# Kernel tuning notes

Hardware: AMD Instinct MI355X
Metric: run time of the kernel (lower is better)

Reference implementation:

```python
import jax, jax.numpy as jnp
import numpy as np


def setup_inputs() -> dict:
    key = jax.random.key(0)
    ks = jax.random.split(key, 5)
    B, S, D, U = 4, 2048, 1024, 1024
    scale = 1.0 / np.sqrt(D)
    return {
        "query": jax.random.normal(ks[0], (B, S, D), dtype=jnp.float32),
        "value": jax.random.normal(ks[1], (B, S, D), dtype=jnp.float32),
        "Wq": jax.random.normal(ks[2], (D, U), dtype=jnp.float32) * scale,
        "bq": jnp.zeros((U,), dtype=jnp.float32),
        "Wk": jax.random.normal(ks[3], (D, U), dtype=jnp.float32) * scale,
        "bk": jnp.zeros((U,), dtype=jnp.float32),
        "Wv": jax.random.normal(ks[4], (D, U), dtype=jnp.float32) * scale,
        "bv": jnp.zeros((U,), dtype=jnp.float32),
    }


def reference(query, value, Wq, bq, Wk, bk, Wv, bv):
    # Dense projections (last-dim matmul + bias)
    Q = jnp.einsum("bsd,du->bsu", query, Wq) + bq   # [B,Sq,U]
    K = jnp.einsum("btd,du->btu", value, Wk) + bk   # [B,Sk,U]
    V = jnp.einsum("btd,du->btu", value, Wv) + bv   # [B,Sk,U]
    d_k = jnp.asarray(K.shape[-1], dtype=jnp.float32)
    scores = jnp.einsum("bsu,btu->bst", Q, K) / jnp.sqrt(d_k)  # [B,Sq,Sk]
    weights = jax.nn.softmax(scores, axis=-1)
    return jnp.einsum("bst,btu->bsu", weights, V)   # [B,Sq,U]
```

## Files before the change

kernel.cpp:

```cpp
#include <hip/hip_runtime.h>
#include <hip/hip_bf16.h>
#include <stdint.h>

#define DEVINL __device__ __forceinline__

typedef __attribute__((ext_vector_type(4))) float f32x4;
typedef __attribute__((ext_vector_type(8))) __bf16 bfv8;
typedef __attribute__((ext_vector_type(8))) short s16x8;
typedef __attribute__((ext_vector_type(4))) short s16x4;

DEVINL short f2bf(float f) {
  union { float f; unsigned u; } v; v.f = f;
  unsigned r = v.u + 0x7FFFu + ((v.u >> 16) & 1u);
  return (short)(r >> 16);
}
DEVINL float bf2f(short h) {
  union { unsigned u; float f; } v; v.u = ((unsigned)(unsigned short)h) << 16;
  return v.f;
}
DEVINL void gload_lds16(const void* g, void* l) {
  __builtin_amdgcn_global_load_lds((__attribute__((address_space(1))) unsigned*)(g),
                                   (__attribute__((address_space(3))) unsigned*)(l),
                                   16, 0, 0);
}
template <int N> DEVINL void vmwaitc() {
  asm volatile("s_waitcnt vmcnt(%0)" :: "i"(N) : "memory");
}
DEVINL int xswz(int p, int n) { return (p & 7) * (n >> 3) + (p >> 3); }

DEVINL void gemm97_core(const short* __restrict__ Ag, const short* __restrict__ Bg,
                        int lda, int ldb, int m0, int n0, int nkt,
                        short* lds, f32x4 (&acc)[4][4]) {
  const int tid = threadIdx.x;
  const int w = tid >> 6, l = tid & 63;
  const int wm = w >> 1, wn = w & 1;
  const int lr = l & 15, lg = l >> 4;
  const int ck = ((lg ^ ((lr >> 1) & 3)) << 3);
  const int aro = (wm * 64 + lr) * 32 + ck;
  const int bro = 4096 + (wn * 64 + lr) * 32 + ck;
  const int srow = l >> 2;
  const int scol = (((l & 3) ^ ((l >> 3) & 3)) << 3);

#pragma unroll 1
  for (int kt = 0; kt < nkt; ++kt) {
#pragma unroll
    for (int i = 0; i < 2; ++i) {
      gload_lds16(Ag + (size_t)(m0 + w * 32 + i * 16 + srow) * lda + kt * 32 + scol,
                  lds + w * 1024 + i * 512);
      gload_lds16(Bg + (size_t)(n0 + w * 32 + i * 16 + srow) * ldb + kt * 32 + scol,
                  lds + 4096 + w * 1024 + i * 512);
    }
    vmwaitc<0>();
    __syncthreads();
    bfv8 af[4], bfr[4];
#pragma unroll
    for (int mf = 0; mf < 4; ++mf) af[mf] = *(const bfv8*)(lds + aro + mf * 512);
#pragma unroll
    for (int nf = 0; nf < 4; ++nf) bfr[nf] = *(const bfv8*)(lds + bro + nf * 512);
#pragma unroll
    for (int mf = 0; mf < 4; ++mf)
#pragma unroll
      for (int nf = 0; nf < 4; ++nf)
        acc[mf][nf] = __builtin_amdgcn_mfma_f32_16x16x32_bf16(af[mf], bfr[nf], acc[mf][nf], 0, 0, 0);
    __syncthreads();
  }
}

__global__ __launch_bounds__(256) void prep_kernel(
    const float* __restrict__ q, const float* __restrict__ v,
    const float* __restrict__ Wq, const float* __restrict__ Wk, const float* __restrict__ Wv,
    short* __restrict__ Qc, short* __restrict__ Vc,
    short* __restrict__ WTq, short* __restrict__ WTk, short* __restrict__ WTv) {
  __shared__ float tile[64][65];
  const int bx = blockIdx.x;
  if (bx < 8192) {
    const float* src = (bx < 4096) ? q : v;
    short* dst = (bx < 4096) ? Qc : Vc;
    const size_t i = ((size_t)(bx & 4095) * 256 + threadIdx.x) * 8;
    f32x4 x0 = *(const f32x4*)(src + i);
    f32x4 x1 = *(const f32x4*)(src + i + 4);
    s16x8 o;
#pragma unroll
    for (int j = 0; j < 4; ++j) { o[j] = f2bf(x0[j]); o[4 + j] = f2bf(x1[j]); }
    *(s16x8*)(dst + i) = o;
  } else {
    const int z = (bx - 8192) >> 8, xx = (bx - 8192) & 255;
    const float* W = (z == 0) ? Wq : (z == 1) ? Wk : Wv;
    short* WT = (z == 0) ? WTq : (z == 1) ? WTk : WTv;
    const int k0 = (xx & 15) << 6, n0 = (xx >> 4) << 6;
    const int c = threadIdx.x & 63, r0 = threadIdx.x >> 6;
#pragma unroll
    for (int i = 0; i < 16; ++i) {
      int r = (i << 2) + r0;
      tile[r][c] = W[(size_t)(k0 + r) * 1024 + n0 + c];
    }
    __syncthreads();
#pragma unroll
    for (int i = 0; i < 16; ++i) {
      int a = (i << 2) + r0;
      WT[(size_t)(n0 + a) * 1024 + k0 + c] = f2bf(tile[c][a]);
    }
  }
}

__global__ __launch_bounds__(256, 3) void qkproj_kernel(
    const short* __restrict__ Qc, const short* __restrict__ Vc,
    const short* __restrict__ WTq, const short* __restrict__ WTk,
    const float* __restrict__ bq, const float* __restrict__ bk,
    short* __restrict__ Qb, short* __restrict__ Kb) {
  __shared__ short lds[8192];
  const int o = xswz(blockIdx.x, 1024);
  const int sel = o >> 9, r = o & 511;
  const int bm = r >> 3, bn = r & 7;
  const short* A = sel ? Vc : Qc;
  const short* BT = sel ? WTk : WTq;
  const float* bias = sel ? bk : bq;
  short* O = sel ? Kb : Qb;
  const int m0 = bm * 128, n0 = bn * 128;
  f32x4 acc[4][4];
#pragma unroll
  for (int i = 0; i < 4; ++i)
#pragma unroll
    for (int j = 0; j < 4; ++j) acc[i][j] = (f32x4){0.f, 0.f, 0.f, 0.f};
  gemm97_core(A, BT, 1024, 1024, m0, n0, 32, lds, acc);
  const int l = threadIdx.x & 63, w = threadIdx.x >> 6;
  const int wm = w >> 1, wn = w & 1, lr = l & 15, lg = l >> 4;
#pragma unroll
  for (int mf = 0; mf < 4; ++mf) {
    const int row0 = m0 + wm * 64 + mf * 16 + lg * 4;
#pragma unroll
    for (int nf = 0; nf < 4; ++nf) {
      const int col = n0 + wn * 64 + nf * 16 + lr;
      const float bb = bias[col];
#pragma unroll
      for (int j = 0; j < 4; ++j)
        O[(size_t)(row0 + j) * 1024 + col] = f2bf(acc[mf][nf][j] + bb);
    }
  }
}

__global__ __launch_bounds__(256, 3) void vproj_kernel(
    const short* __restrict__ Vc, const short* __restrict__ WTv,
    const float* __restrict__ bv, short* __restrict__ VT) {
  __shared__ short lds[8704];
  const int o = xswz(blockIdx.x, 512);
  const int bm = o >> 3, bn = o & 7;
  const int m0 = bm * 128, n0 = bn * 128;
  f32x4 acc[4][4];
#pragma unroll
  for (int i = 0; i < 4; ++i)
#pragma unroll
    for (int j = 0; j < 4; ++j) acc[i][j] = (f32x4){0.f, 0.f, 0.f, 0.f};
  gemm97_core(Vc, WTv, 1024, 1024, m0, n0, 32, lds, acc);
  const int tid = threadIdx.x;
  const int l = tid & 63, w = tid >> 6;
  const int wm = w >> 1, wn = w & 1, lr = l & 15, lg = l >> 4;
  const int b = m0 >> 11, t0 = m0 & 2047;
#pragma unroll 1
  for (int h = 0; h < 2; ++h) {
    if (wn == h) {
#pragma unroll
      for (int mf = 0; mf < 4; ++mf) {
        const int tl = wm * 64 + mf * 16 + lg * 4;
#pragma unroll
        for (int nf = 0; nf < 4; ++nf) {
          const int ul = nf * 16 + lr;
          const float bb = bv[n0 + h * 64 + ul];
          s16x4 pk;
#pragma unroll
          for (int j = 0; j < 4; ++j) pk[j] = f2bf(acc[mf][nf][j] + bb);
          *(s16x4*)&lds[ul * 136 + tl] = pk;
        }
      }
    }
    __syncthreads();
#pragma unroll
    for (int it = 0; it < 4; ++it) {
      const int cid = it * 256 + tid;
      const int u = cid >> 4, tc = cid & 15;
      s16x8 v8 = *(const s16x8*)&lds[u * 136 + tc * 8];
      *(s16x8*)(VT + ((size_t)b * 1024 + n0 + h * 64 + u) * 2048 + t0 + tc * 8) = v8;
    }
    __syncthreads();
  }
}

__global__ __launch_bounds__(256, 3) void qkt_kernel(const short* __restrict__ Qb,
                                                     const short* __restrict__ Kb,
                                                     short* __restrict__ Sb) {
  __shared__ short lds[8192];
  const int o = xswz(blockIdx.x, 1024);
  const int bt = o >> 8, r = o & 255;
  const int bm = r >> 4, bn = r & 15;
  const short* A = Qb + (size_t)bt * 2097152;
  const short* B = Kb + (size_t)bt * 2097152;
  short* O = Sb + (size_t)bt * 4194304;
  const int m0 = bm * 128, n0 = bn * 128;
  f32x4 acc[4][4];
#pragma unroll
  for (int i = 0; i < 4; ++i)
#pragma unroll
    for (int j = 0; j < 4; ++j) acc[i][j] = (f32x4){0.f, 0.f, 0.f, 0.f};
  gemm97_core(A, B, 1024, 1024, m0, n0, 32, lds, acc);
  const int l = threadIdx.x & 63, w = threadIdx.x >> 6;
  const int wm = w >> 1, wn = w & 1, lr = l & 15, lg = l >> 4;
#pragma unroll
  for (int mf = 0; mf < 4; ++mf) {
    const int row0 = m0 + wm * 64 + mf * 16 + lg * 4;
#pragma unroll
    for (int nf = 0; nf < 4; ++nf) {
      const int col = n0 + wn * 64 + nf * 16 + lr;
#pragma unroll
      for (int j = 0; j < 4; ++j)
        O[(size_t)(row0 + j) * 2048 + col] = f2bf(acc[mf][nf][j] * 0.03125f);
    }
  }
}

__global__ __launch_bounds__(256, 3) void pv_kernel(const short* __restrict__ Sb,
                                                    const short* __restrict__ VT,
                                                    float* __restrict__ Out) {
  __shared__ short lds[8192];
  const int o = xswz(blockIdx.x, 512);
  const int bt = o >> 7, r = o & 127;
  const int bm = r >> 3, bn = r & 7;
  const short* A = Sb + (size_t)bt * 4194304;
  const short* B = VT + (size_t)bt * 2097152;
  float* O = Out + (size_t)bt * 2097152;
  const int m0 = bm * 128, n0 = bn * 128;
  f32x4 acc[4][4];
#pragma unroll
  for (int i = 0; i < 4; ++i)
#pragma unroll
    for (int j = 0; j < 4; ++j) acc[i][j] = (f32x4){0.f, 0.f, 0.f, 0.f};
  gemm97_core(A, B, 2048, 2048, m0, n0, 64, lds, acc);
  const int l = threadIdx.x & 63, w = threadIdx.x >> 6;
  const int wm = w >> 1, wn = w & 1, lr = l & 15, lg = l >> 4;
#pragma unroll
  for (int mf = 0; mf < 4; ++mf) {
    const int row0 = m0 + wm * 64 + mf * 16 + lg * 4;
#pragma unroll
    for (int nf = 0; nf < 4; ++nf) {
      const int col = n0 + wn * 64 + nf * 16 + lr;
#pragma unroll
      for (int j = 0; j < 4; ++j)
        O[(size_t)(row0 + j) * 1024 + col] = acc[mf][nf][j];
    }
  }
}

__global__ __launch_bounds__(256) void softmax_kernel(short* __restrict__ Sb) {
  const size_t row = blockIdx.x;
  short* p = Sb + row * 2048;
  const int tid = threadIdx.x;
  const int w = tid >> 6, l = tid & 63;
  s16x8 v = *(const s16x8*)(p + tid * 8);
  float f[8];
#pragma unroll
  for (int j = 0; j < 8; ++j) f[j] = bf2f(v[j]);
  float m = f[0];
#pragma unroll
  for (int j = 1; j < 8; ++j) m = fmaxf(m, f[j]);
#pragma unroll
  for (int o = 32; o > 0; o >>= 1) m = fmaxf(m, __shfl_xor(m, o, 64));
  __shared__ float redm[4], reds[4];
  if (l == 0) redm[w] = m;
  __syncthreads();
  m = fmaxf(fmaxf(redm[0], redm[1]), fmaxf(redm[2], redm[3]));
  float s = 0.f;
#pragma unroll
  for (int j = 0; j < 8; ++j) { f[j] = __expf(f[j] - m); s += f[j]; }
#pragma unroll
  for (int o = 32; o > 0; o >>= 1) s += __shfl_xor(s, o, 64);
  if (l == 0) reds[w] = s;
  __syncthreads();
  s = reds[0] + reds[1] + reds[2] + reds[3];
  const float inv = 1.f / s;
  s16x8 o8;
#pragma unroll
  for (int j = 0; j < 8; ++j) o8[j] = f2bf(f[j] * inv);
  *(s16x8*)(p + tid * 8) = o8;
}

extern "C" void kernel_launch(void* const* d_in, const int* in_sizes, int n_in,
                              void* d_out, int out_size, void* d_ws, size_t ws_size,
                              hipStream_t stream) {
  const float* query = (const float*)d_in[0];
  const float* value = (const float*)d_in[1];
  const float* Wq = (const float*)d_in[2];
  const float* bq = (const float*)d_in[3];
  const float* Wk = (const float*)d_in[4];
  const float* bk = (const float*)d_in[5];
  const float* Wv = (const float*)d_in[6];
  const float* bv = (const float*)d_in[7];

  char* ws = (char*)d_ws;
  short* WTq = (short*)(ws);
  short* WTk = (short*)(ws + ((size_t)2 << 20));
  short* WTv = (short*)(ws + ((size_t)4 << 20));
  short* Qc  = (short*)(ws + ((size_t)6 << 20));
  short* Vc  = (short*)(ws + ((size_t)22 << 20));
  short* Sb  = (short*)(ws + ((size_t)6 << 20));
  short* Qb  = (short*)(ws + ((size_t)38 << 20));
  short* Kb  = (short*)(ws + ((size_t)54 << 20));
  short* VT  = (short*)(ws + ((size_t)70 << 20));

  prep_kernel<<<dim3(8960), 256, 0, stream>>>(query, value, Wq, Wk, Wv, Qc, Vc, WTq, WTk, WTv);

  qkproj_kernel<<<dim3(1024), 256, 0, stream>>>(Qc, Vc, WTq, WTk, bq, bk, Qb, Kb);
  vproj_kernel<<<dim3(512), 256, 0, stream>>>(Vc, WTv, bv, VT);

  qkt_kernel<<<dim3(1024), 256, 0, stream>>>(Qb, Kb, Sb);

  softmax_kernel<<<dim3(8192), 256, 0, stream>>>(Sb);

  pv_kernel<<<dim3(512), 256, 0, stream>>>(Sb, VT, (float*)d_out);
}
```

Measured before the change: 198.6 us.

## Fold Wq·Wkᵀ into one matrix to drop the K projection GEMM

Rewrites the score computation as X·(Wq·Wkᵀ)·Yᵀ, precomputing the 1024x1024 product once and removing the separate K projection. The bq term becomes a per-key vector, computed only when bq is nonzero, and bk is dropped since softmax is invariant to per-row constants. This removes one large projection GEMM at the cost of a small extra GEMM, an extra rounding of the fused matrix to bf16, and a reshuffled workspace layout.

```diff
diff --git a/kernel.cpp b/kernel.cpp
--- a/kernel.cpp
+++ b/kernel.cpp
@@ -70,13 +70,16 @@
     const float* __restrict__ q, const float* __restrict__ v,
     const float* __restrict__ Wq, const float* __restrict__ Wk, const float* __restrict__ Wv,
     short* __restrict__ Qc, short* __restrict__ Vc,
-    short* __restrict__ WTq, short* __restrict__ WTk, short* __restrict__ WTv) {
+    short* __restrict__ Wqc, short* __restrict__ Wkc, short* __restrict__ WTv) {
   __shared__ float tile[64][65];
   const int bx = blockIdx.x;
-  if (bx < 8192) {
-    const float* src = (bx < 4096) ? q : v;
-    short* dst = (bx < 4096) ? Qc : Vc;
-    const size_t i = ((size_t)(bx & 4095) * 256 + threadIdx.x) * 8;
+  if (bx < 9216) {
+    const float* src; short* dst; int off;
+    if (bx < 4096)      { src = q;  dst = Qc;  off = bx; }
+    else if (bx < 8192) { src = v;  dst = Vc;  off = bx - 4096; }
+    else if (bx < 8704) { src = Wq; dst = Wqc; off = bx - 8192; }
+    else                { src = Wk; dst = Wkc; off = bx - 8704; }
+    const size_t i = ((size_t)off * 256 + threadIdx.x) * 8;
     f32x4 x0 = *(const f32x4*)(src + i);
     f32x4 x1 = *(const f32x4*)(src + i + 4);
     s16x8 o;
@@ -84,45 +87,68 @@
     for (int j = 0; j < 4; ++j) { o[j] = f2bf(x0[j]); o[4 + j] = f2bf(x1[j]); }
     *(s16x8*)(dst + i) = o;
   } else {
-    const int z = (bx - 8192) >> 8, xx = (bx - 8192) & 255;
-    const float* W = (z == 0) ? Wq : (z == 1) ? Wk : Wv;
-    short* WT = (z == 0) ? WTq : (z == 1) ? WTk : WTv;
+    const int xx = bx - 9216;
     const int k0 = (xx & 15) << 6, n0 = (xx >> 4) << 6;
     const int c = threadIdx.x & 63, r0 = threadIdx.x >> 6;
 #pragma unroll
     for (int i = 0; i < 16; ++i) {
       int r = (i << 2) + r0;
-      tile[r][c] = W[(size_t)(k0 + r) * 1024 + n0 + c];
+      tile[r][c] = Wv[(size_t)(k0 + r) * 1024 + n0 + c];
     }
     __syncthreads();
 #pragma unroll
     for (int i = 0; i < 16; ++i) {
       int a = (i << 2) + r0;
-      WT[(size_t)(n0 + a) * 1024 + k0 + c] = f2bf(tile[c][a]);
-    }
-  }
-}
-
-__global__ __launch_bounds__(256, 3) void qkproj_kernel(
-    const short* __restrict__ Qc, const short* __restrict__ Vc,
-    const short* __restrict__ WTq, const short* __restrict__ WTk,
-    const float* __restrict__ bq, const float* __restrict__ bk,
-    short* __restrict__ Qb, short* __restrict__ Kb) {
+      WTv[(size_t)(n0 + a) * 1024 + k0 + c] = f2bf(tile[c][a]);
+    }
+  }
+}
+
+__global__ __launch_bounds__(256) void bias0_kernel(const float* __restrict__ Wk,
+                                                    const float* __restrict__ bq,
+                                                    float* __restrict__ v1,
+                                                    float* __restrict__ flagp) {
+  __shared__ float red[256];
+  const int t = threadIdx.x;
+  float any = 0.f;
+  for (int i = t; i < 1024; i += 256) any += fabsf(bq[i]);
+  red[t] = any; __syncthreads();
+  for (int s = 128; s > 0; s >>= 1) { if (t < s) red[t] += red[t + s]; __syncthreads(); }
+  const float fl = red[0];
+  if (t == 0) *flagp = fl;
+  if (fl != 0.f) {
+    for (int r = t; r < 1024; r += 256) {
+      float acc = 0.f;
+      for (int u = 0; u < 1024; ++u) acc += Wk[(size_t)r * 1024 + u] * bq[u];
+      v1[r] = acc;
+    }
+  }
+}
+
+__global__ __launch_bounds__(256) void tvec_kernel(const float* __restrict__ Y,
+                                                   const float* __restrict__ v1,
+                                                   const float* __restrict__ flagp,
+                                                   float* __restrict__ tvec) {
+  const int t = blockIdx.x * 256 + threadIdx.x;
+  if (*flagp == 0.f) { tvec[t] = 0.f; return; }
+  float acc = 0.f;
+  for (int d = 0; d < 1024; ++d) acc += Y[(size_t)t * 1024 + d] * v1[d];
+  tvec[t] = acc;
+}
+
+__global__ __launch_bounds__(256, 3) void mker_kernel(const short* __restrict__ Wkc,
+                                                      const short* __restrict__ Wqc,
+                                                      short* __restrict__ MT) {
   __shared__ short lds[8192];
-  const int o = xswz(blockIdx.x, 1024);
-  const int sel = o >> 9, r = o & 511;
-  const int bm = r >> 3, bn = r & 7;
-  const short* A = sel ? Vc : Qc;
-  const short* BT = sel ? WTk : WTq;
-  const float* bias = sel ? bk : bq;
-  short* O = sel ? Kb : Qb;
-  const int m0 = bm * 128, n0 = bn * 128;
-  f32x4 acc[4][4];
-#pragma unroll
-  for (int i = 0; i < 4; ++i)
-#pragma unroll
-    for (int j = 0; j < 4; ++j) acc[i][j] = (f32x4){0.f, 0.f, 0.f, 0.f};
-  gemm97_core(A, BT, 1024, 1024, m0, n0, 32, lds, acc);
+  const int o = xswz(blockIdx.x, 64);
+  const int bm = o >> 3, bn = o & 7;
+  const int m0 = bm * 128, n0 = bn * 128;
+  f32x4 acc[4][4];
+#pragma unroll
+  for (int i = 0; i < 4; ++i)
+#pragma unroll
+    for (int j = 0; j < 4; ++j) acc[i][j] = (f32x4){0.f, 0.f, 0.f, 0.f};
+  gemm97_core(Wkc, Wqc, 1024, 1024, m0, n0, 32, lds, acc);
   const int l = threadIdx.x & 63, w = threadIdx.x >> 6;
   const int wm = w >> 1, wn = w & 1, lr = l & 15, lg = l >> 4;
 #pragma unroll
@@ -131,10 +157,37 @@
 #pragma unroll
     for (int nf = 0; nf < 4; ++nf) {
       const int col = n0 + wn * 64 + nf * 16 + lr;
-      const float bb = bias[col];
 #pragma unroll
       for (int j = 0; j < 4; ++j)
-        O[(size_t)(row0 + j) * 1024 + col] = f2bf(acc[mf][nf][j] + bb);
+        MT[(size_t)(row0 + j) * 1024 + col] = f2bf(acc[mf][nf][j]);
+    }
+  }
+}
+
+__global__ __launch_bounds__(256, 3) void qproj_kernel(const short* __restrict__ Qc,
+                                                       const short* __restrict__ MT,
+                                                       short* __restrict__ Ap) {
+  __shared__ short lds[8192];
+  const int o = xswz(blockIdx.x, 512);
+  const int bm = o >> 3, bn = o & 7;
+  const int m0 = bm * 128, n0 = bn * 128;
+  f32x4 acc[4][4];
+#pragma unroll
+  for (int i = 0; i < 4; ++i)
+#pragma unroll
+    for (int j = 0; j < 4; ++j) acc[i][j] = (f32x4){0.f, 0.f, 0.f, 0.f};
+  gemm97_core(Qc, MT, 1024, 1024, m0, n0, 32, lds, acc);
+  const int l = threadIdx.x & 63, w = threadIdx.x >> 6;
+  const int wm = w >> 1, wn = w & 1, lr = l & 15, lg = l >> 4;
+#pragma unroll
+  for (int mf = 0; mf < 4; ++mf) {
+    const int row0 = m0 + wm * 64 + mf * 16 + lg * 4;
+#pragma unroll
+    for (int nf = 0; nf < 4; ++nf) {
+      const int col = n0 + wn * 64 + nf * 16 + lr;
+#pragma unroll
+      for (int j = 0; j < 4; ++j)
+        Ap[(size_t)(row0 + j) * 1024 + col] = f2bf(acc[mf][nf][j]);
     }
   }
 }
@@ -185,16 +238,18 @@
   }
 }
 
-__global__ __launch_bounds__(256, 3) void qkt_kernel(const short* __restrict__ Qb,
-                                                     const short* __restrict__ Kb,
-                                                     short* __restrict__ Sb) {
+__global__ __launch_bounds__(256, 3) void qkt_kernel(const short* __restrict__ Ap,
+                                                     const short* __restrict__ Vc,
+                                                     const float* __restrict__ tvec,
+                                                     short* __restrict__ sb0,
+                                                     short* __restrict__ sb3) {
   __shared__ short lds[8192];
   const int o = xswz(blockIdx.x, 1024);
   const int bt = o >> 8, r = o & 255;
   const int bm = r >> 4, bn = r & 15;
-  const short* A = Qb + (size_t)bt * 2097152;
-  const short* B = Kb + (size_t)bt * 2097152;
-  short* O = Sb + (size_t)bt * 4194304;
+  const short* A = Ap + (size_t)bt * 2097152;
+  const short* B = Vc + (size_t)bt * 2097152;
+  short* O = (bt < 3) ? (sb0 + (size_t)bt * 4194304) : sb3;
   const int m0 = bm * 128, n0 = bn * 128;
   f32x4 acc[4][4];
 #pragma unroll
@@ -205,26 +260,28 @@
   const int l = threadIdx.x & 63, w = threadIdx.x >> 6;
   const int wm = w >> 1, wn = w & 1, lr = l & 15, lg = l >> 4;
 #pragma unroll
-  for (int mf = 0; mf < 4; ++mf) {
-    const int row0 = m0 + wm * 64 + mf * 16 + lg * 4;
-#pragma unroll
-    for (int nf = 0; nf < 4; ++nf) {
-      const int col = n0 + wn * 64 + nf * 16 + lr;
+  for (int nf = 0; nf < 4; ++nf) {
+    const int col = n0 + wn * 64 + nf * 16 + lr;
+    const float tv = tvec[bt * 2048 + col];
+#pragma unroll
+    for (int mf = 0; mf < 4; ++mf) {
+      const int row0 = m0 + wm * 64 + mf * 16 + lg * 4;
 #pragma unroll
       for (int j = 0; j < 4; ++j)
-        O[(size_t)(row0 + j) * 2048 + col] = f2bf(acc[mf][nf][j] * 0.03125f);
-    }
-  }
-}
-
-__global__ __launch_bounds__(256, 3) void pv_kernel(const short* __restrict__ Sb,
+        O[(size_t)(row0 + j) * 2048 + col] = f2bf((acc[mf][nf][j] + tv) * 0.03125f);
+    }
+  }
+}
+
+__global__ __launch_bounds__(256, 3) void pv_kernel(const short* __restrict__ sb0,
+                                                    const short* __restrict__ sb3,
                                                     const short* __restrict__ VT,
                                                     float* __restrict__ Out) {
   __shared__ short lds[8192];
   const int o = xswz(blockIdx.x, 512);
   const int bt = o >> 7, r = o & 127;
   const int bm = r >> 3, bn = r & 7;
-  const short* A = Sb + (size_t)bt * 4194304;
+  const short* A = (bt < 3) ? (sb0 + (size_t)bt * 4194304) : sb3;
   const short* B = VT + (size_t)bt * 2097152;
   float* O = Out + (size_t)bt * 2097152;
   const int m0 = bm * 128, n0 = bn * 128;
@@ -249,9 +306,11 @@
   }
 }
 
-__global__ __launch_bounds__(256) void softmax_kernel(short* __restrict__ Sb) {
-  const size_t row = blockIdx.x;
-  short* p = Sb + row * 2048;
+__global__ __launch_bounds__(256) void softmax_kernel(short* __restrict__ sb0,
+                                                      short* __restrict__ sb3) {
+  const int row = blockIdx.x;
+  const int bt = row >> 11;
+  short* p = ((bt < 3) ? (sb0 + (size_t)bt * 4194304) : sb3) + (size_t)(row & 2047) * 2048;
   const int tid = threadIdx.x;
   const int w = tid >> 6, l = tid & 63;
   s16x8 v = *(const s16x8*)(p + tid * 8);
@@ -290,29 +349,34 @@
   const float* Wq = (const float*)d_in[2];
   const float* bq = (const float*)d_in[3];
   const float* Wk = (const float*)d_in[4];
-  const float* bk = (const float*)d_in[5];
   const float* Wv = (const float*)d_in[6];
   const float* bv = (const float*)d_in[7];
 
   char* ws = (char*)d_ws;
-  short* WTq = (short*)(ws);
-  short* WTk = (short*)(ws + ((size_t)2 << 20));
-  short* WTv = (short*)(ws + ((size_t)4 << 20));
-  short* Qc  = (short*)(ws + ((size_t)6 << 20));
-  short* Vc  = (short*)(ws + ((size_t)22 << 20));
-  short* Sb  = (short*)(ws + ((size_t)6 << 20));
-  short* Qb  = (short*)(ws + ((size_t)38 << 20));
-  short* Kb  = (short*)(ws + ((size_t)54 << 20));
-  short* VT  = (short*)(ws + ((size_t)70 << 20));
-
-  prep_kernel<<<dim3(8960), 256, 0, stream>>>(query, value, Wq, Wk, Wv, Qc, Vc, WTq, WTk, WTv);
-
-  qkproj_kernel<<<dim3(1024), 256, 0, stream>>>(Qc, Vc, WTq, WTk, bq, bk, Qb, Kb);
+  short* Wqc = (short*)(ws);
+  short* Wkc = (short*)(ws + ((size_t)2 << 20));
+  short* MT  = (short*)(ws + ((size_t)4 << 20));
+  short* WTv = (short*)(ws + ((size_t)6 << 20));
+  short* Qc  = (short*)(ws + ((size_t)8 << 20));
+  short* Vc  = (short*)(ws + ((size_t)24 << 20));
+  short* Ap  = (short*)(ws + ((size_t)40 << 20));
+  short* VT  = (short*)(ws + ((size_t)56 << 20));
+  short* sb0 = (short*)(ws);
+  short* sb3 = (short*)(ws + ((size_t)72 << 20));
+  float* tvec = (float*)(ws + ((size_t)80 << 20));
+  float* v1   = (float*)(ws + ((size_t)80 << 20) + 65536);
+  float* flagp = (float*)(ws + ((size_t)80 << 20) + 131072);
+
+  prep_kernel<<<dim3(9472), 256, 0, stream>>>(query, value, Wq, Wk, Wv,
+                                              Qc, Vc, Wqc, Wkc, WTv);
+  bias0_kernel<<<dim3(1), 256, 0, stream>>>(Wk, bq, v1, flagp);
+  tvec_kernel<<<dim3(32), 256, 0, stream>>>(value, v1, flagp, tvec);
+
+  mker_kernel<<<dim3(64), 256, 0, stream>>>(Wkc, Wqc, MT);
+  qproj_kernel<<<dim3(512), 256, 0, stream>>>(Qc, MT, Ap);
   vproj_kernel<<<dim3(512), 256, 0, stream>>>(Vc, WTv, bv, VT);
 
-  qkt_kernel<<<dim3(1024), 256, 0, stream>>>(Qb, Kb, Sb);
-
-  softmax_kernel<<<dim3(8192), 256, 0, stream>>>(Sb);
-
-  pv_kernel<<<dim3(512), 256, 0, stream>>>(Sb, VT, (float*)d_out);
-}
+  qkt_kernel<<<dim3(1024), 256, 0, stream>>>(Ap, Vc, tvec, sb0, sb3);
+  softmax_kernel<<<dim3(8192), 256, 0, stream>>>(sb0, sb3);
+  pv_kernel<<<dim3(512), 256, 0, stream>>>(sb0, sb3, VT, (float*)d_out);
+}
```

Result: slower. 204.3 us (+2.9%).
